# Kernel optimization log

Hardware: AMD Instinct MI355X
Metric: run time of the kernel (lower is better)

The kernel has to match this reference:

```python
import jax, jax.numpy as jnp
import numpy as np

N_NODES = 100000
N_EDGES = 800000
NUM_GRAPHS = 64


def _lin_init(key, fan_in, fan_out):
    k1, k2 = jax.random.split(key)
    s = 1.0 / np.sqrt(fan_in)
    W = jax.random.uniform(k1, (fan_in, fan_out), jnp.float32, -s, s)
    b = jax.random.uniform(k2, (fan_out,), jnp.float32, -s, s)
    return W, b


def setup_inputs() -> dict:
    key = jax.random.key(0)
    ks = jax.random.split(key, 20)
    inp = {
        'x1': jax.random.normal(ks[0], (N_NODES, 384), jnp.float32),
        'x2': jax.random.normal(ks[1], (N_NODES, 32), jnp.float32),
        'pe': jax.random.normal(ks[2], (N_NODES, 64), jnp.float32),
        'edge_index': jax.random.randint(ks[3], (2, N_EDGES), 0, N_NODES, jnp.int32),
        'batch': jnp.sort(jax.random.randint(ks[4], (N_NODES,), 0, NUM_GRAPHS, jnp.int32)),
    }
    # parameters (fan_in, fan_out) per __init__ dims
    inp['Wc'], inp['bc'] = _lin_init(ks[5], 384, 192)     # embed_contraction
    inp['Wmf'], inp['bmf'] = _lin_init(ks[6], 192, 256)   # mpnn_feature
    inp['Wgf'], inp['bgf'] = _lin_init(ks[7], 256, 192)   # gcn_feature
    inp['Wmc'], inp['bmc'] = _lin_init(ks[8], 32, 64)     # mpnn_class
    inp['Wgc'], inp['bgc'] = _lin_init(ks[9], 64, 192)    # gcn_class
    inp['Wa1'], inp['ba1'] = _lin_init(ks[10], 192, 256)  # attention_nn[0]
    inp['Wa2'], inp['ba2'] = _lin_init(ks[11], 256, 192)  # attention_nn[2]
    inp['Wgd'], inp['bgd'] = _lin_init(ks[12], 192, 192)  # gcn_decoder
    inp['Wd1'], inp['bd1'] = _lin_init(ks[13], 192, 192)  # mpnn_decoder1
    inp['Wd2'], inp['bd2'] = _lin_init(ks[14], 192, 192)  # mpnn_decoder2
    inp['Wd3'], inp['bd3'] = _lin_init(ks[15], 192, 384)  # mpnn_decoder3
    return inp


def _mpnn(x, src, dst, W, b):
    # aggr='add': scatter-add gathered source features to targets, then Linear
    agg = jax.ops.segment_sum(x[src], dst, num_segments=N_NODES)
    return agg @ W + b


def _gcn(x, src, dst, W, b):
    # GCNConv with default self-loops and symmetric deg^-1/2 normalization
    h = x @ W
    deg = jax.ops.segment_sum(jnp.ones(src.shape[0], h.dtype), dst, num_segments=N_NODES) + 1.0
    dinv = jax.lax.rsqrt(deg)
    norm = dinv[src] * dinv[dst]
    agg = jax.ops.segment_sum(h[src] * norm[:, None], dst, num_segments=N_NODES)
    agg = agg + h * (dinv * dinv)[:, None]  # self-loop contribution
    return agg + b


def reference(x1, x2, pe, edge_index, batch,
              Wc, bc, Wmf, bmf, Wgf, bgf, Wmc, bmc, Wgc, bgc,
              Wa1, ba1, Wa2, ba2, Wgd, bgd, Wd1, bd1, Wd2, bd2, Wd3, bd3):
    src, dst = edge_index[0], edge_index[1]
    pe3 = jnp.concatenate([pe, pe, pe], axis=-1)  # [N, 192]

    # ---- encoder ----
    x1_res = jax.nn.relu(x1 @ Wc + bc)            # [N, 192]
    h = x1_res + pe3
    h = jax.nn.relu(_mpnn(h, src, dst, Wmf, bmf))  # [N, 256]
    h = jax.nn.relu(_gcn(h, src, dst, Wgf, bgf))   # [N, 192]
    c = jax.nn.relu(_mpnn(x2, src, dst, Wmc, bmc)) # [N, 64]
    c = jax.nn.relu(_gcn(c, src, dst, Wgc, bgc))   # [N, 192]
    z = h + c + x1_res

    # attentional aggregation: gate = attention_nn(z), segment softmax, weighted sum
    gate = jax.nn.relu(z @ Wa1 + ba1) @ Wa2 + ba2   # [N, 192]
    gmax = jax.ops.segment_max(gate, batch, num_segments=NUM_GRAPHS)
    e = jnp.exp(gate - gmax[batch])
    esum = jax.ops.segment_sum(e, batch, num_segments=NUM_GRAPHS)
    alpha = e / esum[batch]
    zg = jax.ops.segment_sum(alpha * z, batch, num_segments=NUM_GRAPHS)  # [B, 192]

    # ---- decoder ----
    z1 = zg[batch]                                  # broadcast graph embedding to nodes
    z1_res = jax.nn.relu(_gcn(z1, src, dst, Wgd, bgd))
    t = z1_res + pe3
    t = jax.nn.relu(_mpnn(t, src, dst, Wd1, bd1))
    t = jax.nn.relu(_mpnn(t, src, dst, Wd2, bd2)) + z1_res
    out = jax.nn.relu(_mpnn(t, src, dst, Wd3, bd3))  # [N, 384]
    return out
```

## Files before the change

kernel.cpp:

```cpp
#include <hip/hip_runtime.h>
#include <math.h>

#define N_NODES 100000
#define N_EDGES 800000
#define NGRAPH  64

typedef __attribute__((ext_vector_type(8))) __bf16 bf16x8;
typedef __attribute__((ext_vector_type(4))) float f32x4;

static __device__ __forceinline__ unsigned flip_f(float x) {
  unsigned u = __float_as_uint(x);
  return u ^ ((u & 0x80000000u) ? 0xFFFFFFFFu : 0x80000000u);
}
static __device__ __forceinline__ float unflip_f(unsigned m) {
  unsigned u = m ^ ((m & 0x80000000u) ? 0x80000000u : 0xFFFFFFFFu);
  return __uint_as_float(u);
}
static __device__ __forceinline__ unsigned short f2bf(float x) {
  unsigned u = __float_as_uint(x);
  u += 0x7fffu + ((u >> 16) & 1u);
  return (unsigned short)(u >> 16);
}
static __device__ __forceinline__ unsigned pk2(float a, float b) {
  return (unsigned)f2bf(a) | ((unsigned)f2bf(b) << 16);
}
static __device__ __forceinline__ float bf2f(unsigned short h) {
  return __uint_as_float((unsigned)h << 16);
}
static __device__ __forceinline__ void unpack8(uint4 w, float* f) {
  f[0] = __uint_as_float(w.x << 16); f[1] = __uint_as_float(w.x & 0xFFFF0000u);
  f[2] = __uint_as_float(w.y << 16); f[3] = __uint_as_float(w.y & 0xFFFF0000u);
  f[4] = __uint_as_float(w.z << 16); f[5] = __uint_as_float(w.z & 0xFFFF0000u);
  f[6] = __uint_as_float(w.w << 16); f[7] = __uint_as_float(w.w & 0xFFFF0000u);
}
static __device__ __forceinline__ uint4 pack8(const float* f) {
  uint4 w;
  w.x = pk2(f[0], f[1]); w.y = pk2(f[2], f[3]);
  w.z = pk2(f[4], f[5]); w.w = pk2(f[6], f[7]);
  return w;
}

__global__ void hist_k(const int* __restrict__ dst, int* __restrict__ cnt) {
  int e = blockIdx.x * 256 + threadIdx.x;
  if (e < N_EDGES) atomicAdd(&cnt[dst[e]], 1);
}

__global__ void dinv_k(const int* __restrict__ cnt, float* __restrict__ dinv) {
  int i = blockIdx.x * 256 + threadIdx.x;
  if (i < N_NODES) dinv[i] = rsqrtf((float)cnt[i] + 1.0f);
}

__global__ void scan_block_k(const int* __restrict__ cnt, int* __restrict__ rs,
                             int* __restrict__ bsum) {
  __shared__ int s[256];
  int t = threadIdx.x, i = blockIdx.x * 256 + t;
  int v = (i < N_NODES) ? cnt[i] : 0;
  s[t] = v; __syncthreads();
  for (int off = 1; off < 256; off <<= 1) {
    int a = (t >= off) ? s[t - off] : 0;
    __syncthreads();
    s[t] += a;
    __syncthreads();
  }
  if (i < N_NODES) rs[i] = s[t] - v;
  if (t == 255) bsum[blockIdx.x] = s[255];
}

__global__ void scan_bsum_k(int* __restrict__ bsum, int nb) {
  __shared__ int s[512];
  int t = threadIdx.x;
  int v = (t < nb) ? bsum[t] : 0;
  s[t] = v; __syncthreads();
  for (int off = 1; off < 512; off <<= 1) {
    int a = (t >= off) ? s[t - off] : 0;
    __syncthreads();
    s[t] += a;
    __syncthreads();
  }
  if (t < nb) bsum[t] = s[t] - v;
}

__global__ void scan_add_k(int* __restrict__ rs, int* __restrict__ cursor,
                           const int* __restrict__ bsum) {
  int i = blockIdx.x * 256 + threadIdx.x;
  if (i < N_NODES) {
    int r = rs[i] + bsum[i >> 8];
    rs[i] = r;
    cursor[i] = r;
  }
}

__global__ void build_k(const int* __restrict__ src, const int* __restrict__ dst,
                        int* __restrict__ cursor, int* __restrict__ srcs) {
  int e = blockIdx.x * 256 + threadIdx.x;
  if (e < N_EDGES) {
    int d = dst[e];
    int p = atomicAdd(&cursor[d], 1);
    srcs[p] = src[e];
  }
}

__global__ void graph_starts_k(const int* __restrict__ batch, int* __restrict__ gstart) {
  int g = threadIdx.x;
  if (g > NGRAPH) return;
  if (g == NGRAPH) { gstart[NGRAPH] = N_NODES; return; }
  int lo = 0, hi = N_NODES;
  while (lo < hi) {
    int mid = (lo + hi) >> 1;
    if (batch[mid] < g) lo = mid + 1; else hi = mid;
  }
  gstart[g] = lo;
}

template <typename AT, int MT, int NT, bool OUT_F32>
__global__ __launch_bounds__(256)
void gemm_t(const AT* __restrict__ A, const float* __restrict__ B,
            const float* __restrict__ bias,
            const unsigned short* __restrict__ add1,
            const unsigned short* __restrict__ add2,
            void* __restrict__ Cv, int M, int K, int F, int relu) {
  constexpr int BM = 64 * MT;
  constexpr int BN = 16 * NT;
  __shared__ unsigned short As[BM * 40];
  __shared__ unsigned short Bs[BN * 40];
  const int tid = threadIdx.x;
  const int wave = tid >> 6, lane = tid & 63;
  const int quad = lane >> 4, l16 = lane & 15;
  const int row0 = blockIdx.x * BM;
  const int col0 = blockIdx.y * BN;

  f32x4 acc[MT][NT];
#pragma unroll
  for (int i = 0; i < MT; i++)
#pragma unroll
    for (int j = 0; j < NT; j++) acc[i][j] = (f32x4){0.f, 0.f, 0.f, 0.f};

  for (int k0 = 0; k0 < K; k0 += 32) {
    if (k0) __syncthreads();
    if constexpr (sizeof(AT) == 4) {
      int ar = tid >> 1, ah = (tid & 1) * 16;
      int row = row0 + ar;
      uint4 w0 = make_uint4(0, 0, 0, 0), w1 = w0;
      if (row < M) {
        const float* ap = (const float*)A + (size_t)row * K + k0 + ah;
        float4 v0 = *(const float4*)(ap + 0);
        float4 v1 = *(const float4*)(ap + 4);
        float4 v2 = *(const float4*)(ap + 8);
        float4 v3 = *(const float4*)(ap + 12);
        w0.x = pk2(v0.x, v0.y); w0.y = pk2(v0.z, v0.w);
        w0.z = pk2(v1.x, v1.y); w0.w = pk2(v1.z, v1.w);
        w1.x = pk2(v2.x, v2.y); w1.y = pk2(v2.z, v2.w);
        w1.z = pk2(v3.x, v3.y); w1.w = pk2(v3.z, v3.w);
      }
      *(uint4*)&As[ar * 40 + ah] = w0;
      *(uint4*)&As[ar * 40 + ah + 8] = w1;
    } else if constexpr (MT == 2) {
      int ar = tid >> 1, ah = (tid & 1) * 16;
      int row = row0 + ar;
      uint4 w0 = make_uint4(0, 0, 0, 0), w1 = w0;
      if (row < M) {
        const unsigned short* ap = (const unsigned short*)A + (size_t)row * K + k0 + ah;
        w0 = *(const uint4*)ap;
        w1 = *(const uint4*)(ap + 8);
      }
      *(uint4*)&As[ar * 40 + ah] = w0;
      *(uint4*)&As[ar * 40 + ah + 8] = w1;
    } else {
      int ar = tid >> 2, ap4 = (tid & 3) * 8;
      int row = row0 + ar;
      uint4 w = make_uint4(0, 0, 0, 0);
      if (row < M)
        w = *(const uint4*)((const unsigned short*)A + (size_t)row * K + k0 + ap4);
      *(uint4*)&As[ar * 40 + ap4] = w;
    }
#pragma unroll
    for (int c = 0; c < NT / 4; c++) {
      int bn = tid & 63, bkk = (tid >> 6) * 8;
      int col = col0 + c * 64 + bn;
      const float* bp = B + (size_t)(k0 + bkk) * F + col;
      uint4 w;
      w.x = pk2(bp[0 * F], bp[1 * F]); w.y = pk2(bp[2 * F], bp[3 * F]);
      w.z = pk2(bp[4 * F], bp[5 * F]); w.w = pk2(bp[6 * F], bp[7 * F]);
      *(uint4*)&Bs[(c * 64 + bn) * 40 + bkk] = w;
    }
    __syncthreads();

    bf16x8 af[MT], bfr[NT];
#pragma unroll
    for (int mt = 0; mt < MT; mt++) {
      int m = wave * (MT * 16) + mt * 16 + l16;
      af[mt] = *(bf16x8*)&As[m * 40 + quad * 8];
    }
#pragma unroll
    for (int nt = 0; nt < NT; nt++) {
      int n = nt * 16 + l16;
      bfr[nt] = *(bf16x8*)&Bs[n * 40 + quad * 8];
    }
#pragma unroll
    for (int mt = 0; mt < MT; mt++)
#pragma unroll
      for (int nt = 0; nt < NT; nt++)
        acc[mt][nt] = __builtin_amdgcn_mfma_f32_16x16x32_bf16(af[mt], bfr[nt], acc[mt][nt], 0, 0, 0);
  }

  float* Cf = (float*)Cv;
  unsigned short* Ch = (unsigned short*)Cv;
#pragma unroll
  for (int mt = 0; mt < MT; mt++) {
#pragma unroll
    for (int r = 0; r < 4; r++) {
      int row = row0 + wave * (MT * 16) + mt * 16 + quad * 4 + r;
      if (row >= M) continue;
#pragma unroll
      for (int nt = 0; nt < NT; nt++) {
        int col = col0 + nt * 16 + l16;
        float v = acc[mt][nt][r];
        if (bias) v += bias[col];
        if (relu) v = fmaxf(v, 0.f);
        size_t off = (size_t)row * F + col;
        if (add1) v += bf2f(add1[off]);
        if (add2) v += bf2f(add2[off]);
        if (OUT_F32) Cf[off] = v; else Ch[off] = f2bf(v);
      }
    }
  }
}

__global__ __launch_bounds__(256)
void gemm_kernel(const float* __restrict__ A, const float* __restrict__ B,
                 const float* __restrict__ bias, float* __restrict__ C,
                 int M, int K, int F) {
  __shared__ float Asm[16][65];
  __shared__ float Bsm[16][65];
  const int tid = threadIdx.x;
  const int tx = tid & 15, ty = tid >> 4;
  const int row0 = blockIdx.x * 64;
  const int col0 = blockIdx.y * 64;
  float acc[4][4];
#pragma unroll
  for (int i = 0; i < 4; i++)
#pragma unroll
    for (int j = 0; j < 4; j++) acc[i][j] = 0.f;

  for (int k0 = 0; k0 < K; k0 += 16) {
#pragma unroll
    for (int l = 0; l < 4; l++) {
      int idx = tid + l * 256;
      int m = idx >> 4, k = idx & 15;
      int r = row0 + m;
      Asm[k][m] = (r < M) ? A[(size_t)r * K + k0 + k] : 0.f;
    }
#pragma unroll
    for (int l = 0; l < 4; l++) {
      int idx = tid + l * 256;
      int k = idx >> 6, n = idx & 63;
      Bsm[k][n] = B[(size_t)(k0 + k) * F + col0 + n];
    }
    __syncthreads();
#pragma unroll
    for (int k = 0; k < 16; k++) {
      float a[4], b[4];
#pragma unroll
      for (int i = 0; i < 4; i++) a[i] = Asm[k][ty * 4 + i];
#pragma unroll
      for (int j = 0; j < 4; j++) b[j] = Bsm[k][tx * 4 + j];
#pragma unroll
      for (int i = 0; i < 4; i++)
#pragma unroll
        for (int j = 0; j < 4; j++) acc[i][j] += a[i] * b[j];
    }
    __syncthreads();
  }
#pragma unroll
  for (int i = 0; i < 4; i++) {
    int r = row0 + ty * 4 + i;
    if (r >= M) continue;
#pragma unroll
    for (int j = 0; j < 4; j++) {
      int c = col0 + tx * 4 + j;
      float v = acc[i][j];
      if (bias) v += bias[c];
      C[(size_t)r * F + c] = v;
    }
  }
}

__global__ void add_pe3_bf(const unsigned short* __restrict__ a, const float* __restrict__ pe,
                           unsigned short* __restrict__ out) {
  int t = blockIdx.x * 256 + threadIdx.x;
  if (t >= N_NODES * 24) return;
  int i = t / 24, c = (t - i * 24) * 8;
  uint4 w = *(const uint4*)(a + (size_t)i * 192 + c);
  float f[8]; unpack8(w, f);
  const float* p = pe + (size_t)i * 64 + (c & 63);
#pragma unroll
  for (int j = 0; j < 8; j++) f[j] += p[j];
  *(uint4*)(out + (size_t)i * 192 + c) = pack8(f);
}

template <int F>
__global__ void agg_mpnn_bf(const unsigned short* __restrict__ x, const int* __restrict__ rowstart,
                            const int* __restrict__ cnt, const int* __restrict__ srcs,
                            unsigned short* __restrict__ out) {
  constexpr int F8 = F / 8;
  int t = blockIdx.x * 256 + threadIdx.x;
  if (t >= N_NODES * F8) return;
  int i = t / F8, c = (t - i * F8) * 8;
  float a[8] = {0.f, 0.f, 0.f, 0.f, 0.f, 0.f, 0.f, 0.f};
  int e = rowstart[i], e1 = e + cnt[i];
  for (; e < e1; ++e) {
    int s = srcs[e];
    uint4 w = *(const uint4*)(x + (size_t)s * F + c);
    float f[8]; unpack8(w, f);
#pragma unroll
    for (int j = 0; j < 8; j++) a[j] += f[j];
  }
  *(uint4*)(out + (size_t)i * F + c) = pack8(a);
}

template <int F, bool RELU, bool HAS_BIAS>
__global__ void agg_gcn_bf(const unsigned short* __restrict__ x, const int* __restrict__ rowstart,
                           const int* __restrict__ cnt, const int* __restrict__ srcs,
                           const float* __restrict__ dinv, const float* __restrict__ bias,
                           unsigned short* __restrict__ out) {
  constexpr int F8 = F / 8;
  int t = blockIdx.x * 256 + threadIdx.x;
  if (t >= N_NODES * F8) return;
  int i = t / F8, c = (t - i * F8) * 8;
  float a[8] = {0.f, 0.f, 0.f, 0.f, 0.f, 0.f, 0.f, 0.f};
  int e = rowstart[i], e1 = e + cnt[i];
  for (; e < e1; ++e) {
    int s = srcs[e];
    float w = dinv[s];
    uint4 wv = *(const uint4*)(x + (size_t)s * F + c);
    float f[8]; unpack8(wv, f);
#pragma unroll
    for (int j = 0; j < 8; j++) a[j] += w * f[j];
  }
  float di = dinv[i];
  float sw = di * di;
  uint4 sv = *(const uint4*)(x + (size_t)i * F + c);
  float sf[8]; unpack8(sv, sf);
  float r[8];
#pragma unroll
  for (int j = 0; j < 8; j++) {
    float v = di * a[j] + sw * sf[j];
    if (HAS_BIAS) v += bias[c + j];
    if (RELU) v = fmaxf(v, 0.f);
    r[j] = v;
  }
  *(uint4*)(out + (size_t)i * F + c) = pack8(r);
}

__global__ void agg_x2_k(const float* __restrict__ x, const int* __restrict__ rowstart,
                         const int* __restrict__ cnt, const int* __restrict__ srcs,
                         unsigned short* __restrict__ out) {
  int t = blockIdx.x * 256 + threadIdx.x;
  if (t >= N_NODES * 8) return;
  int i = t >> 3, c = (t & 7) * 4;
  float4 acc = make_float4(0.f, 0.f, 0.f, 0.f);
  int e = rowstart[i], e1 = e + cnt[i];
  for (; e < e1; ++e) {
    int s = srcs[e];
    float4 v = *(const float4*)(x + (size_t)s * 32 + c);
    acc.x += v.x; acc.y += v.y; acc.z += v.z; acc.w += v.w;
  }
  ushort4 o;
  o.x = f2bf(acc.x); o.y = f2bf(acc.y); o.z = f2bf(acc.z); o.w = f2bf(acc.w);
  *(ushort4*)(out + (size_t)i * 32 + c) = o;
}

__global__ void agg_gcn_dec_bf(const float* __restrict__ zgW, const int* __restrict__ rowstart,
                               const int* __restrict__ cnt, const int* __restrict__ srcs,
                               const int* __restrict__ batch, const float* __restrict__ dinv,
                               const float* __restrict__ bias, unsigned short* __restrict__ out) {
  int t = blockIdx.x * 256 + threadIdx.x;
  if (t >= N_NODES * 24) return;
  int i = t / 24, c = (t - i * 24) * 8;
  float a[8] = {0.f, 0.f, 0.f, 0.f, 0.f, 0.f, 0.f, 0.f};
  int e = rowstart[i], e1 = e + cnt[i];
  for (; e < e1; ++e) {
    int s = srcs[e];
    float w = dinv[s];
    const float* v = zgW + (size_t)batch[s] * 192 + c;
#pragma unroll
    for (int j = 0; j < 8; j++) a[j] += w * v[j];
  }
  float di = dinv[i];
  float sw = di * di;
  const float* sv = zgW + (size_t)batch[i] * 192 + c;
  float r[8];
#pragma unroll
  for (int j = 0; j < 8; j++)
    r[j] = fmaxf(di * a[j] + sw * sv[j] + bias[c + j], 0.f);
  *(uint4*)(out + (size_t)i * 192 + c) = pack8(r);
}

__global__ void init_gmax_k(unsigned* __restrict__ gmaxu) {
  int t = blockIdx.x * 256 + threadIdx.x;
  if (t < NGRAPH * 192) gmaxu[t] = 0x007FFFFFu;
}

__global__ void seg_max_k(const float* __restrict__ gate, const int* __restrict__ gstart,
                          unsigned* __restrict__ gmaxu) {
  int g = blockIdx.x, f = threadIdx.x;
  int lo = gstart[g], hi = gstart[g + 1];
  int len = hi - lo;
  if (len <= 0) return;
  int per = (len + gridDim.y - 1) / gridDim.y;
  int a = lo + blockIdx.y * per;
  int b = min(a + per, hi);
  if (a >= b) return;
  float m = -INFINITY;
  for (int i = a; i < b; i++) m = fmaxf(m, gate[(size_t)i * 192 + f]);
  atomicMax(&gmaxu[g * 192 + f], flip_f(m));
}

__global__ void seg_sum_k(const float* __restrict__ gate, const unsigned short* __restrict__ z,
                          const int* __restrict__ gstart, const unsigned* __restrict__ gmaxu,
                          float* __restrict__ esum, float* __restrict__ znum) {
  int g = blockIdx.x, f = threadIdx.x;
  int lo = gstart[g], hi = gstart[g + 1];
  int len = hi - lo;
  if (len <= 0) return;
  int per = (len + gridDim.y - 1) / gridDim.y;
  int a = lo + blockIdx.y * per;
  int b = min(a + per, hi);
  if (a >= b) return;
  float gm = unflip_f(gmaxu[g * 192 + f]);
  float se = 0.f, sz = 0.f;
  for (int i = a; i < b; i++) {
    float e = expf(gate[(size_t)i * 192 + f] - gm);
    se += e;
    sz += e * bf2f(z[(size_t)i * 192 + f]);
  }
  atomicAdd(&esum[g * 192 + f], se);
  atomicAdd(&znum[g * 192 + f], sz);
}

__global__ void zg_fin_k(const float* __restrict__ znum, const float* __restrict__ esum,
                         float* __restrict__ zg) {
  int t = blockIdx.x * 256 + threadIdx.x;
  if (t >= NGRAPH * 192) return;
  float es = esum[t];
  zg[t] = (es > 0.f) ? znum[t] / es : 0.f;
}

extern "C" void kernel_launch(void* const* d_in, const int* in_sizes, int n_in,
                              void* d_out, int out_size, void* d_ws, size_t ws_size,
                              hipStream_t stream) {
  const float* x1 = (const float*)d_in[0];
  const float* x2 = (const float*)d_in[1];
  const float* pe = (const float*)d_in[2];
  const int* ei = (const int*)d_in[3];
  const int* src = ei;
  const int* dst = ei + N_EDGES;
  const int* batch = (const int*)d_in[4];
  const float* Wc  = (const float*)d_in[5];  const float* bc  = (const float*)d_in[6];
  const float* Wmf = (const float*)d_in[7];  const float* bmf = (const float*)d_in[8];
  const float* Wgf = (const float*)d_in[9];  const float* bgf = (const float*)d_in[10];
  const float* Wmc = (const float*)d_in[11]; const float* bmc = (const float*)d_in[12];
  const float* Wgc = (const float*)d_in[13]; const float* bgc = (const float*)d_in[14];
  const float* Wa1 = (const float*)d_in[15]; const float* ba1 = (const float*)d_in[16];
  const float* Wa2 = (const float*)d_in[17]; const float* ba2 = (const float*)d_in[18];
  const float* Wgd = (const float*)d_in[19]; const float* bgd = (const float*)d_in[20];
  const float* Wd1 = (const float*)d_in[21]; const float* bd1 = (const float*)d_in[22];
  const float* Wd2 = (const float*)d_in[23]; const float* bd2 = (const float*)d_in[24];
  const float* Wd3 = (const float*)d_in[25]; const float* bd3 = (const float*)d_in[26];
  float* out = (float*)d_out;

  char* base = (char*)d_ws;
  size_t woff = 0;
  auto walloc = [&](size_t bytes) -> void* {
    void* p = base + woff;
    woff = (woff + bytes + 255) & ~(size_t)255;
    return p;
  };
  unsigned short* P0h = (unsigned short*)walloc((size_t)N_NODES * 192 * 2);
  unsigned short* P1h = (unsigned short*)walloc((size_t)N_NODES * 256 * 2);
  unsigned short* P2h = (unsigned short*)walloc((size_t)N_NODES * 192 * 2);
  unsigned short* P5a = (unsigned short*)walloc((size_t)N_NODES * 32 * 2);
  unsigned short* P5b = (unsigned short*)walloc((size_t)N_NODES * 64 * 2);
  unsigned short* P5c = (unsigned short*)walloc((size_t)N_NODES * 64 * 2);
  float* Pg   = (float*)walloc((size_t)N_NODES * 192 * 4);
  float* dinv = (float*)walloc((size_t)N_NODES * 4);
  unsigned* gmaxu = (unsigned*)walloc((size_t)NGRAPH * 192 * 4);
  float* esum = (float*)walloc((size_t)NGRAPH * 192 * 4);
  float* znum = (float*)walloc((size_t)NGRAPH * 192 * 4);
  float* zg   = (float*)walloc((size_t)NGRAPH * 192 * 4);
  float* zgW  = (float*)walloc((size_t)NGRAPH * 192 * 4);
  int* cnt      = (int*)walloc((size_t)N_NODES * 4);
  int* rowstart = (int*)walloc((size_t)N_NODES * 4);
  int* cursor   = (int*)walloc((size_t)N_NODES * 4);
  int* srcs     = (int*)walloc((size_t)N_EDGES * 4);
  int* bsum     = (int*)walloc(512 * 4);
  int* gstart   = (int*)walloc(80 * 4);

  unsigned short* P3h = (unsigned short*)d_out;
  unsigned short* P4h = (unsigned short*)((float*)d_out + (size_t)N_NODES * 192);

  const int TB = 256;
  hipMemsetAsync(cnt, 0, N_NODES * sizeof(int), stream);
  hipMemsetAsync(esum, 0, 2 * NGRAPH * 192 * sizeof(float), stream);

  hist_k<<<(N_EDGES + TB - 1) / TB, TB, 0, stream>>>(dst, cnt);
  dinv_k<<<(N_NODES + TB - 1) / TB, TB, 0, stream>>>(cnt, dinv);
  int nb = (N_NODES + 255) / 256;
  scan_block_k<<<nb, 256, 0, stream>>>(cnt, rowstart, bsum);
  scan_bsum_k<<<1, 512, 0, stream>>>(bsum, nb);
  scan_add_k<<<nb, 256, 0, stream>>>(rowstart, cursor, bsum);
  build_k<<<(N_EDGES + TB - 1) / TB, TB, 0, stream>>>(src, dst, cursor, srcs);
  graph_starts_k<<<1, 128, 0, stream>>>(batch, gstart);

  const int mb128 = (N_NODES + 127) / 128;
  const int mb64 = (N_NODES + 63) / 64;
  const int ew24 = (N_NODES * 24 + TB - 1) / TB;
  const int ew8 = (N_NODES * 8 + TB - 1) / TB;

  gemm_t<float, 2, 12, false><<<mb128, 256, 0, stream>>>(x1, Wc, bc, nullptr, nullptr, P0h, N_NODES, 384, 192, 1);
  add_pe3_bf<<<ew24, TB, 0, stream>>>(P0h, pe, P1h);
  agg_mpnn_bf<192><<<ew24, TB, 0, stream>>>(P1h, rowstart, cnt, srcs, P2h);
  gemm_t<unsigned short, 1, 16, false><<<mb64, 256, 0, stream>>>(P2h, Wmf, bmf, nullptr, nullptr, P1h, N_NODES, 192, 256, 1);
  gemm_t<unsigned short, 2, 12, false><<<mb128, 256, 0, stream>>>(P1h, Wgf, nullptr, nullptr, nullptr, P3h, N_NODES, 256, 192, 0);
  agg_gcn_bf<192, true, true><<<ew24, TB, 0, stream>>>(P3h, rowstart, cnt, srcs, dinv, bgf, P4h);
  agg_x2_k<<<ew8, TB, 0, stream>>>(x2, rowstart, cnt, srcs, P5a);
  gemm_t<unsigned short, 2, 4, false><<<mb128, 256, 0, stream>>>(P5a, Wmc, bmc, nullptr, nullptr, P5b, N_NODES, 32, 64, 1);
  agg_gcn_bf<64, false, false><<<ew8, TB, 0, stream>>>(P5b, rowstart, cnt, srcs, dinv, nullptr, P5c);
  gemm_t<unsigned short, 2, 12, false><<<mb128, 256, 0, stream>>>(P5c, Wgc, bgc, P4h, P0h, P0h, N_NODES, 64, 192, 1);

  gemm_t<unsigned short, 1, 16, false><<<mb64, 256, 0, stream>>>(P0h, Wa1, ba1, nullptr, nullptr, P1h, N_NODES, 192, 256, 1);
  gemm_t<unsigned short, 2, 12, true><<<mb128, 256, 0, stream>>>(P1h, Wa2, ba2, nullptr, nullptr, Pg, N_NODES, 256, 192, 0);
  init_gmax_k<<<(NGRAPH * 192 + TB - 1) / TB, TB, 0, stream>>>(gmaxu);
  dim3 sg(NGRAPH, 16);
  seg_max_k<<<sg, 192, 0, stream>>>(Pg, gstart, gmaxu);
  seg_sum_k<<<sg, 192, 0, stream>>>(Pg, P0h, gstart, gmaxu, esum, znum);
  zg_fin_k<<<(NGRAPH * 192 + TB - 1) / TB, TB, 0, stream>>>(znum, esum, zg);
  gemm_kernel<<<dim3(1, 3), 256, 0, stream>>>(zg, Wgd, nullptr, zgW, NGRAPH, 192, 192);

  agg_gcn_dec_bf<<<ew24, TB, 0, stream>>>(zgW, rowstart, cnt, srcs, batch, dinv, bgd, P4h);
  add_pe3_bf<<<ew24, TB, 0, stream>>>(P4h, pe, P2h);
  agg_mpnn_bf<192><<<ew24, TB, 0, stream>>>(P2h, rowstart, cnt, srcs, P3h);
  gemm_t<unsigned short, 2, 12, false><<<mb128, 256, 0, stream>>>(P3h, Wd1, bd1, nullptr, nullptr, P1h, N_NODES, 192, 192, 1);
  agg_mpnn_bf<192><<<ew24, TB, 0, stream>>>(P1h, rowstart, cnt, srcs, P2h);
  gemm_t<unsigned short, 2, 12, false><<<mb128, 256, 0, stream>>>(P2h, Wd2, bd2, P4h, nullptr, P3h, N_NODES, 192, 192, 1);
  agg_mpnn_bf<192><<<ew24, TB, 0, stream>>>(P3h, rowstart, cnt, srcs, P2h);
  gemm_t<unsigned short, 2, 12, true><<<dim3(mb128, 2), 256, 0, stream>>>(P2h, Wd3, bd3, nullptr, nullptr, out, N_NODES, 192, 384, 1);
  (void)in_sizes; (void)n_in; (void)out_size; (void)ws_size;
}
```

Baseline: 1.651 ms.

## Load A fragments directly to registers and stage whole-K weight tiles in LDS

Replaces the per-32-K tiled GEMM with a kernel that loads A operands straight from global memory into MFMA fragment registers, skipping the LDS staging for A. The B (weight) tile for a large K chunk, or the full K, is converted to bf16 once per block and stored in LDS, which cuts the number of barriers. Tile widths are retuned per layer and some GEMMs are now split across column blocks. In exchange, weights are loaded redundantly across column blocks, LDS per block grows, and the direct A loads are strided per lane, which may coalesce less well.

```diff
diff --git a/kernel.cpp b/kernel.cpp
--- a/kernel.cpp
+++ b/kernel.cpp
@@ -39,6 +39,7 @@
   w.z = pk2(f[4], f[5]); w.w = pk2(f[6], f[7]);
   return w;
 }
+union U4B8 { uint4 u; bf16x8 b; };
 
 __global__ void hist_k(const int* __restrict__ dst, int* __restrict__ cnt) {
   int e = blockIdx.x * 256 + threadIdx.x;
@@ -112,104 +113,90 @@
   gstart[g] = lo;
 }
 
-template <typename AT, int MT, int NT, bool OUT_F32>
+template <typename AT, int K, int KC, int BN, bool OUT_F32>
 __global__ __launch_bounds__(256)
-void gemm_t(const AT* __restrict__ A, const float* __restrict__ B,
-            const float* __restrict__ bias,
-            const unsigned short* __restrict__ add1,
-            const unsigned short* __restrict__ add2,
-            void* __restrict__ Cv, int M, int K, int F, int relu) {
-  constexpr int BM = 64 * MT;
-  constexpr int BN = 16 * NT;
-  __shared__ unsigned short As[BM * 40];
-  __shared__ unsigned short Bs[BN * 40];
+void gemm_ws(const AT* __restrict__ A, const float* __restrict__ B,
+             const float* __restrict__ bias,
+             const unsigned short* __restrict__ add1,
+             const unsigned short* __restrict__ add2,
+             void* __restrict__ Cv, int M, int F, int relu) {
+  constexpr int NC = K / KC;
+  constexpr int KCS = KC / 32;
+  constexpr int NT = BN / 16;
+  constexpr int LDB = KC + 8;
+  constexpr int CH = (BN * KC) / (8 * 256);
+  __shared__ unsigned short Bs[BN * LDB];
+
   const int tid = threadIdx.x;
   const int wave = tid >> 6, lane = tid & 63;
   const int quad = lane >> 4, l16 = lane & 15;
-  const int row0 = blockIdx.x * BM;
   const int col0 = blockIdx.y * BN;
-
-  f32x4 acc[MT][NT];
-#pragma unroll
-  for (int i = 0; i < MT; i++)
-#pragma unroll
-    for (int j = 0; j < NT; j++) acc[i][j] = (f32x4){0.f, 0.f, 0.f, 0.f};
-
-  for (int k0 = 0; k0 < K; k0 += 32) {
-    if (k0) __syncthreads();
-    if constexpr (sizeof(AT) == 4) {
-      int ar = tid >> 1, ah = (tid & 1) * 16;
-      int row = row0 + ar;
-      uint4 w0 = make_uint4(0, 0, 0, 0), w1 = w0;
+  const int rowb = blockIdx.x * 128 + wave * 32;
+
+  f32x4 acc[2][NT];
+#pragma unroll
+  for (int mt = 0; mt < 2; mt++)
+#pragma unroll
+    for (int nt = 0; nt < NT; nt++) acc[mt][nt] = (f32x4){0.f, 0.f, 0.f, 0.f};
+
+  for (int c = 0; c < NC; c++) {
+    if (c) __syncthreads();
+    uint4 afr[2][KCS];
+#pragma unroll
+    for (int mt = 0; mt < 2; mt++) {
+      int row = rowb + mt * 16 + l16;
       if (row < M) {
-        const float* ap = (const float*)A + (size_t)row * K + k0 + ah;
-        float4 v0 = *(const float4*)(ap + 0);
-        float4 v1 = *(const float4*)(ap + 4);
-        float4 v2 = *(const float4*)(ap + 8);
-        float4 v3 = *(const float4*)(ap + 12);
-        w0.x = pk2(v0.x, v0.y); w0.y = pk2(v0.z, v0.w);
-        w0.z = pk2(v1.x, v1.y); w0.w = pk2(v1.z, v1.w);
-        w1.x = pk2(v2.x, v2.y); w1.y = pk2(v2.z, v2.w);
-        w1.z = pk2(v3.x, v3.y); w1.w = pk2(v3.z, v3.w);
+        if constexpr (sizeof(AT) == 4) {
+          const float* ap = (const float*)A + (size_t)row * K + c * KC + quad * 8;
+#pragma unroll
+          for (int ks = 0; ks < KCS; ks++) {
+            float4 u = *(const float4*)(ap + ks * 32);
+            float4 v = *(const float4*)(ap + ks * 32 + 4);
+            afr[mt][ks].x = pk2(u.x, u.y); afr[mt][ks].y = pk2(u.z, u.w);
+            afr[mt][ks].z = pk2(v.x, v.y); afr[mt][ks].w = pk2(v.z, v.w);
+          }
+        } else {
+          const unsigned short* ap = (const unsigned short*)A + (size_t)row * K + c * KC + quad * 8;
+#pragma unroll
+          for (int ks = 0; ks < KCS; ks++) afr[mt][ks] = *(const uint4*)(ap + ks * 32);
+        }
+      } else {
+#pragma unroll
+        for (int ks = 0; ks < KCS; ks++) afr[mt][ks] = make_uint4(0, 0, 0, 0);
       }
-      *(uint4*)&As[ar * 40 + ah] = w0;
-      *(uint4*)&As[ar * 40 + ah + 8] = w1;
-    } else if constexpr (MT == 2) {
-      int ar = tid >> 1, ah = (tid & 1) * 16;
-      int row = row0 + ar;
-      uint4 w0 = make_uint4(0, 0, 0, 0), w1 = w0;
-      if (row < M) {
-        const unsigned short* ap = (const unsigned short*)A + (size_t)row * K + k0 + ah;
-        w0 = *(const uint4*)ap;
-        w1 = *(const uint4*)(ap + 8);
+    }
+#pragma unroll
+    for (int s = 0; s < CH; s++) {
+      int idx = tid + s * 256;
+      int n = idx % BN;
+      int kc = (idx / BN) * 8;
+      const float* bp = B + (size_t)(c * KC + kc) * F + col0 + n;
+      float f[8];
+#pragma unroll
+      for (int j = 0; j < 8; j++) f[j] = bp[(size_t)j * F];
+      *(uint4*)&Bs[n * LDB + kc] = pack8(f);
+    }
+    __syncthreads();
+#pragma unroll
+    for (int ks = 0; ks < KCS; ks++) {
+      U4B8 a0, a1;
+      a0.u = afr[0][ks]; a1.u = afr[1][ks];
+#pragma unroll
+      for (int nt = 0; nt < NT; nt++) {
+        bf16x8 b = *(bf16x8*)&Bs[(nt * 16 + l16) * LDB + ks * 32 + quad * 8];
+        acc[0][nt] = __builtin_amdgcn_mfma_f32_16x16x32_bf16(a0.b, b, acc[0][nt], 0, 0, 0);
+        acc[1][nt] = __builtin_amdgcn_mfma_f32_16x16x32_bf16(a1.b, b, acc[1][nt], 0, 0, 0);
       }
-      *(uint4*)&As[ar * 40 + ah] = w0;
-      *(uint4*)&As[ar * 40 + ah + 8] = w1;
-    } else {
-      int ar = tid >> 2, ap4 = (tid & 3) * 8;
-      int row = row0 + ar;
-      uint4 w = make_uint4(0, 0, 0, 0);
-      if (row < M)
-        w = *(const uint4*)((const unsigned short*)A + (size_t)row * K + k0 + ap4);
-      *(uint4*)&As[ar * 40 + ap4] = w;
-    }
-#pragma unroll
-    for (int c = 0; c < NT / 4; c++) {
-      int bn = tid & 63, bkk = (tid >> 6) * 8;
-      int col = col0 + c * 64 + bn;
-      const float* bp = B + (size_t)(k0 + bkk) * F + col;
-      uint4 w;
-      w.x = pk2(bp[0 * F], bp[1 * F]); w.y = pk2(bp[2 * F], bp[3 * F]);
-      w.z = pk2(bp[4 * F], bp[5 * F]); w.w = pk2(bp[6 * F], bp[7 * F]);
-      *(uint4*)&Bs[(c * 64 + bn) * 40 + bkk] = w;
-    }
-    __syncthreads();
-
-    bf16x8 af[MT], bfr[NT];
-#pragma unroll
-    for (int mt = 0; mt < MT; mt++) {
-      int m = wave * (MT * 16) + mt * 16 + l16;
-      af[mt] = *(bf16x8*)&As[m * 40 + quad * 8];
-    }
-#pragma unroll
-    for (int nt = 0; nt < NT; nt++) {
-      int n = nt * 16 + l16;
-      bfr[nt] = *(bf16x8*)&Bs[n * 40 + quad * 8];
-    }
-#pragma unroll
-    for (int mt = 0; mt < MT; mt++)
-#pragma unroll
-      for (int nt = 0; nt < NT; nt++)
-        acc[mt][nt] = __builtin_amdgcn_mfma_f32_16x16x32_bf16(af[mt], bfr[nt], acc[mt][nt], 0, 0, 0);
+    }
   }
 
   float* Cf = (float*)Cv;
   unsigned short* Ch = (unsigned short*)Cv;
 #pragma unroll
-  for (int mt = 0; mt < MT; mt++) {
+  for (int mt = 0; mt < 2; mt++) {
 #pragma unroll
     for (int r = 0; r < 4; r++) {
-      int row = row0 + wave * (MT * 16) + mt * 16 + quad * 4 + r;
+      int row = rowb + mt * 16 + quad * 4 + r;
       if (row >= M) continue;
 #pragma unroll
       for (int nt = 0; nt < NT; nt++) {
@@ -220,7 +207,7 @@
         size_t off = (size_t)row * F + col;
         if (add1) v += bf2f(add1[off]);
         if (add2) v += bf2f(add2[off]);
-        if (OUT_F32) Cf[off] = v; else Ch[off] = f2bf(v);
+        if constexpr (OUT_F32) Cf[off] = v; else Ch[off] = f2bf(v);
       }
     }
   }
@@ -512,24 +499,23 @@
   build_k<<<(N_EDGES + TB - 1) / TB, TB, 0, stream>>>(src, dst, cursor, srcs);
   graph_starts_k<<<1, 128, 0, stream>>>(batch, gstart);
 
-  const int mb128 = (N_NODES + 127) / 128;
-  const int mb64 = (N_NODES + 63) / 64;
+  const int gmt = (N_NODES + 127) / 128;
   const int ew24 = (N_NODES * 24 + TB - 1) / TB;
   const int ew8 = (N_NODES * 8 + TB - 1) / TB;
 
-  gemm_t<float, 2, 12, false><<<mb128, 256, 0, stream>>>(x1, Wc, bc, nullptr, nullptr, P0h, N_NODES, 384, 192, 1);
+  gemm_ws<float, 384, 128, 192, false><<<dim3(gmt, 1), 256, 0, stream>>>(x1, Wc, bc, nullptr, nullptr, P0h, N_NODES, 192, 1);
   add_pe3_bf<<<ew24, TB, 0, stream>>>(P0h, pe, P1h);
   agg_mpnn_bf<192><<<ew24, TB, 0, stream>>>(P1h, rowstart, cnt, srcs, P2h);
-  gemm_t<unsigned short, 1, 16, false><<<mb64, 256, 0, stream>>>(P2h, Wmf, bmf, nullptr, nullptr, P1h, N_NODES, 192, 256, 1);
-  gemm_t<unsigned short, 2, 12, false><<<mb128, 256, 0, stream>>>(P1h, Wgf, nullptr, nullptr, nullptr, P3h, N_NODES, 256, 192, 0);
+  gemm_ws<unsigned short, 192, 192, 128, false><<<dim3(gmt, 2), 256, 0, stream>>>(P2h, Wmf, bmf, nullptr, nullptr, P1h, N_NODES, 256, 1);
+  gemm_ws<unsigned short, 256, 256, 96, false><<<dim3(gmt, 2), 256, 0, stream>>>(P1h, Wgf, nullptr, nullptr, nullptr, P3h, N_NODES, 192, 0);
   agg_gcn_bf<192, true, true><<<ew24, TB, 0, stream>>>(P3h, rowstart, cnt, srcs, dinv, bgf, P4h);
   agg_x2_k<<<ew8, TB, 0, stream>>>(x2, rowstart, cnt, srcs, P5a);
-  gemm_t<unsigned short, 2, 4, false><<<mb128, 256, 0, stream>>>(P5a, Wmc, bmc, nullptr, nullptr, P5b, N_NODES, 32, 64, 1);
+  gemm_ws<unsigned short, 32, 32, 64, false><<<dim3(gmt, 1), 256, 0, stream>>>(P5a, Wmc, bmc, nullptr, nullptr, P5b, N_NODES, 64, 1);
   agg_gcn_bf<64, false, false><<<ew8, TB, 0, stream>>>(P5b, rowstart, cnt, srcs, dinv, nullptr, P5c);
-  gemm_t<unsigned short, 2, 12, false><<<mb128, 256, 0, stream>>>(P5c, Wgc, bgc, P4h, P0h, P0h, N_NODES, 64, 192, 1);
-
-  gemm_t<unsigned short, 1, 16, false><<<mb64, 256, 0, stream>>>(P0h, Wa1, ba1, nullptr, nullptr, P1h, N_NODES, 192, 256, 1);
-  gemm_t<unsigned short, 2, 12, true><<<mb128, 256, 0, stream>>>(P1h, Wa2, ba2, nullptr, nullptr, Pg, N_NODES, 256, 192, 0);
+  gemm_ws<unsigned short, 64, 64, 192, false><<<dim3(gmt, 1), 256, 0, stream>>>(P5c, Wgc, bgc, P4h, P0h, P0h, N_NODES, 192, 1);
+
+  gemm_ws<unsigned short, 192, 192, 128, false><<<dim3(gmt, 2), 256, 0, stream>>>(P0h, Wa1, ba1, nullptr, nullptr, P1h, N_NODES, 256, 1);
+  gemm_ws<unsigned short, 256, 256, 96, true><<<dim3(gmt, 2), 256, 0, stream>>>(P1h, Wa2, ba2, nullptr, nullptr, Pg, N_NODES, 192, 0);
   init_gmax_k<<<(NGRAPH * 192 + TB - 1) / TB, TB, 0, stream>>>(gmaxu);
   dim3 sg(NGRAPH, 16);
   seg_max_k<<<sg, 192, 0, stream>>>(Pg, gstart, gmaxu);
@@ -540,10 +526,10 @@
   agg_gcn_dec_bf<<<ew24, TB, 0, stream>>>(zgW, rowstart, cnt, srcs, batch, dinv, bgd, P4h);
   add_pe3_bf<<<ew24, TB, 0, stream>>>(P4h, pe, P2h);
   agg_mpnn_bf<192><<<ew24, TB, 0, stream>>>(P2h, rowstart, cnt, srcs, P3h);
-  gemm_t<unsigned short, 2, 12, false><<<mb128, 256, 0, stream>>>(P3h, Wd1, bd1, nullptr, nullptr, P1h, N_NODES, 192, 192, 1);
+  gemm_ws<unsigned short, 192, 192, 96, false><<<dim3(gmt, 2), 256, 0, stream>>>(P3h, Wd1, bd1, nullptr, nullptr, P1h, N_NODES, 192, 1);
   agg_mpnn_bf<192><<<ew24, TB, 0, stream>>>(P1h, rowstart, cnt, srcs, P2h);
-  gemm_t<unsigned short, 2, 12, false><<<mb128, 256, 0, stream>>>(P2h, Wd2, bd2, P4h, nullptr, P3h, N_NODES, 192, 192, 1);
+  gemm_ws<unsigned short, 192, 192, 96, false><<<dim3(gmt, 2), 256, 0, stream>>>(P2h, Wd2, bd2, P4h, nullptr, P3h, N_NODES, 192, 1);
   agg_mpnn_bf<192><<<ew24, TB, 0, stream>>>(P3h, rowstart, cnt, srcs, P2h);
-  gemm_t<unsigned short, 2, 12, true><<<dim3(mb128, 2), 256, 0, stream>>>(P2h, Wd3, bd3, nullptr, nullptr, out, N_NODES, 192, 384, 1);
+  gemm_ws<unsigned short, 192, 192, 128, true><<<dim3(gmt, 3), 256, 0, stream>>>(P2h, Wd3, bd3, nullptr, nullptr, out, N_NODES, 384, 1);
   (void)in_sizes; (void)n_in; (void)out_size; (void)ws_size;
 }
```

Result: slower. 1.783 ms (+8.0%).
